# Kernel tuning notes

Hardware: AMD Instinct MI355X
Metric: run time of the kernel (lower is better)

## Reference

```python
import jax, jax.numpy as jnp
import numpy as np

B, N, P, HID = 1024, 30, 16, 128
NR = N * (N - 1)          # 870 directed edges
DR, DE, DO, NT = 3, 5, 6, 5


def _lin(x, w, b):
    return x @ w.T + b


def setup_inputs() -> dict:
    key = jax.random.key(0)
    ks = jax.random.split(key, 24)

    def w(k, o, i):
        return jax.random.normal(k, (o, i), jnp.float32) * 0.05

    def bias(k, o):
        return jax.random.normal(k, (o,), jnp.float32) * 0.05

    return {
        "x": jax.random.normal(ks[0], (B, N, P), jnp.float32),
        "RR": jax.random.normal(ks[1], (B, N, NR), jnp.float32),
        "RS": jax.random.normal(ks[2], (B, N, NR), jnp.float32),
        "RA": jax.random.normal(ks[3], (B, DR, NR), jnp.float32),
        "fr1_w": w(ks[4], HID, 2 * P + DR), "fr1_b": bias(ks[5], HID),
        "fr2_w": w(ks[6], HID // 2, HID),   "fr2_b": bias(ks[7], HID // 2),
        "fr3_w": w(ks[8], DE, HID // 2),    "fr3_b": bias(ks[9], DE),
        "fo1_w": w(ks[10], HID, P + DE),    "fo1_b": bias(ks[11], HID),
        "fo2_w": w(ks[12], HID // 2, HID),  "fo2_b": bias(ks[13], HID // 2),
        "fo3_w": w(ks[14], DO, HID // 2),   "fo3_b": bias(ks[15], DO),
        "fc1_w": w(ks[16], HID, DO * N),    "fc1_b": bias(ks[17], HID),
        "fc2_w": w(ks[18], HID // 2, HID),  "fc2_b": bias(ks[19], HID // 2),
        "fc3_w": w(ks[20], NT, HID // 2),   "fc3_b": bias(ks[21], NT),
    }


def reference(x, RR, RS, RA,
              fr1_w, fr1_b, fr2_w, fr2_b, fr3_w, fr3_b,
              fo1_w, fo1_b, fo2_w, fo2_b, fo3_w, fo3_b,
              fc1_w, fc1_b, fc2_w, fc2_b, fc3_w, fc3_b):
    xt = jnp.swapaxes(x, 1, 2)                       # [B, P, N]
    Orr = jnp.einsum('bpn,bnr->bpr', xt, RR)          # [B, P, Nr]
    Ors = jnp.einsum('bpn,bnr->bpr', xt, RS)          # [B, P, Nr]
    Bm = jnp.concatenate([Orr, Ors, RA], axis=1)      # [B, 2P+Dr, Nr]
    Bm = jnp.swapaxes(Bm, 1, 2)                       # [B, Nr, 2P+Dr]
    h = jax.nn.relu(_lin(Bm, fr1_w, fr1_b))
    h = jax.nn.relu(_lin(h, fr2_w, fr2_b))
    E = jax.nn.relu(_lin(h, fr3_w, fr3_b))            # [B, Nr, De]
    Ebar = jnp.einsum('bre,bnr->ben', E, RR)          # E^T @ RR^T -> [B, De, N]
    C = jnp.concatenate([xt, Ebar], axis=1)           # [B, P+De, N]
    C = jnp.swapaxes(C, 1, 2)                         # [B, N, P+De]
    h = jax.nn.relu(_lin(C, fo1_w, fo1_b))
    h = jax.nn.relu(_lin(h, fo2_w, fo2_b))
    O = jax.nn.relu(_lin(h, fo3_w, fo3_b))            # [B, N, Do]
    f = O.reshape(O.shape[0], -1)                     # [B, Do*N]
    f = jax.nn.relu(_lin(f, fc1_w, fc1_b))
    f = jax.nn.relu(_lin(f, fc2_w, fc2_b))
    return _lin(f, fc3_w, fc3_b)                      # [B, n_targets]
```

## Files before the change

kernel.cpp:

```cpp
#include <hip/hip_runtime.h>

#define B_ 1024
#define N_ 30
#define P_ 16
#define NR_ 870
#define DR_ 3
#define DE_ 5
#define DO_ 6
#define NT_ 5

typedef unsigned short ushort_t;
typedef __attribute__((ext_vector_type(8))) short short8_t;
typedef __attribute__((ext_vector_type(4))) float f32x4;

union Frag { short8_t v; ushort_t u[8]; unsigned int d[4]; };

__device__ __forceinline__ float bf2f(ushort_t u) {
    union { unsigned int i; float f; } v; v.i = ((unsigned int)u) << 16; return v.f;
}
__device__ __forceinline__ ushort_t f2bf(float f) {
    union { float f; unsigned int i; } v; v.f = f;
    unsigned int x = v.i;
    return (ushort_t)((x + 0x7FFFu + ((x >> 16) & 1u)) >> 16);
}
__device__ __forceinline__ void split(float v, ushort_t& h, ushort_t& l) {
    h = f2bf(v);
    float r = v - bf2f(h);
    l = f2bf(r);
}
__device__ __forceinline__ unsigned int cvtpk(float a, float b) {
    unsigned int r;
    asm("v_cvt_pk_bf16_f32 %0, %1, %2" : "=v"(r) : "v"(a), "v"(b));
    return r;
}
__device__ __forceinline__ void split2(float a, float b,
                                       unsigned int& h, unsigned int& l) {
    h = cvtpk(a, b);
    union { unsigned int i; float f; } x0, x1;
    x0.i = h << 16; x1.i = h & 0xFFFF0000u;
    l = cvtpk(a - x0.f, b - x1.f);
}
__device__ __forceinline__ f32x4 mfma(short8_t a, short8_t b, f32x4 c) {
    return __builtin_amdgcn_mfma_f32_16x16x32_bf16(a, b, c, 0, 0, 0);
}

__global__ __launch_bounds__(256) void k_prep(
    const float* __restrict__ x,  const float* __restrict__ w1,
    const float* __restrict__ w2, const float* __restrict__ wo1,
    const float* __restrict__ wo2,
    ushort_t* __restrict__ xAh,  ushort_t* __restrict__ xAl,
    ushort_t* __restrict__ w1h,  ushort_t* __restrict__ w1l,
    ushort_t* __restrict__ w2h,  ushort_t* __restrict__ w2l,
    ushort_t* __restrict__ wo1h, ushort_t* __restrict__ wo1l,
    ushort_t* __restrict__ wo2h, ushort_t* __restrict__ wo2l)
{
    const int blk = blockIdx.x, tid = threadIdx.x;
    if (blk < 1024) {
        int b = blk;
        for (int idx = tid; idx < 512; idx += 256) {
            int lane = idx >> 3, j = idx & 7;
            int p = lane & 15, n = (lane >> 4) * 8 + j;
            float v = (n < N_) ? x[(b * N_ + n) * P_ + p] : 0.f;
            ushort_t h_, l_; split(v, h_, l_);
            xAh[b * 512 + idx] = h_; xAl[b * 512 + idx] = l_;
        }
    } else if (blk == 1024) {
        for (int idx = tid; idx < 16 * 512; idx += 256) {
            int f = idx >> 9, eps = idx & 511;
            int lane = eps >> 3, j = eps & 7;
            int mt = f >> 1, kt = f & 1;
            int m = mt * 16 + (lane & 15);
            int k = kt * 32 + (lane >> 4) * 8 + j;
            float v = (k < 35) ? w1[m * 35 + k] : 0.f;
            ushort_t h_, l_; split(v, h_, l_);
            w1h[idx] = h_; w1l[idx] = l_;
        }
    } else if (blk == 1025) {
        for (int idx = tid; idx < 16 * 512; idx += 256) {
            int f = idx >> 9, eps = idx & 511;
            int lane = eps >> 3, j = eps & 7;
            int mt = f >> 2, kt = f & 3;
            int m = mt * 16 + (lane & 15);
            int k = kt * 32 + (lane >> 4) * 8 + j;
            float v = w2[m * 128 + k];
            ushort_t h_, l_; split(v, h_, l_);
            w2h[idx] = h_; w2l[idx] = l_;
        }
    } else if (blk == 1026) {
        for (int idx = tid; idx < 8 * 512; idx += 256) {
            int f = idx >> 9, eps = idx & 511;
            int lane = eps >> 3, j = eps & 7;
            int m = f * 16 + (lane & 15);
            int k = (lane >> 4) * 8 + j;
            float v = (k < 21) ? wo1[m * 21 + k] : 0.f;
            ushort_t h_, l_; split(v, h_, l_);
            wo1h[idx] = h_; wo1l[idx] = l_;
        }
    } else {
        for (int idx = tid; idx < 16 * 512; idx += 256) {
            int f = idx >> 9, eps = idx & 511;
            int lane = eps >> 3, j = eps & 7;
            int mt = f >> 2, kt = f & 3;
            int m = mt * 16 + (lane & 15);
            int k = kt * 32 + (lane >> 4) * 8 + j;
            float v = wo2[m * 128 + k];
            ushort_t h_, l_; split(v, h_, l_);
            wo2h[idx] = h_; wo2l[idx] = l_;
        }
    }
}

__global__ __launch_bounds__(256) void k_edge(
    const float* __restrict__ RR, const float* __restrict__ RS,
    const float* __restrict__ RA,
    const float* __restrict__ b1, const float* __restrict__ b2,
    const float* __restrict__ w3, const float* __restrict__ b3,
    const ushort_t* __restrict__ xAh, const ushort_t* __restrict__ xAl,
    const ushort_t* __restrict__ w1h, const ushort_t* __restrict__ w1l,
    const ushort_t* __restrict__ w2h, const ushort_t* __restrict__ w2l,
    float* __restrict__ Ebar)
{
    const int b   = blockIdx.y;
    const int r0  = blockIdx.x * 64;
    const int tid = threadIdx.x;
    const int lane = tid & 63;
    const int wv   = tid >> 6;
    const int l15  = lane & 15;
    const int q    = lane >> 4;

    __shared__ union {
        ushort_t aT[2][64][72];
        float    h2T[64][68];
    } u1;
    __shared__ ushort_t h1T[2][64][72];
    __shared__ float Ee[64][6];
    __shared__ float b1s[128], b2s[64];

    if (tid < 128) b1s[tid] = b1[tid];
    if (tid < 64)  b2s[tid] = b2[tid];

    const int eloc = wv * 16 + l15;
    const int r = r0 + eloc;
    const bool rvalid = (r < NR_);
    const int rc = rvalid ? r : NR_ - 1;

    {
        Frag xh, xl;
        xh.v = ((const short8_t*)xAh)[b * 64 + lane];
        xl.v = ((const short8_t*)xAl)[b * 64 + lane];

        float vr[8], vs[8];
        #pragma unroll
        for (int j = 0; j < 8; ++j) {
            int n = q * 8 + j;
            vr[j] = (n < N_) ? RR[(b * N_ + n) * NR_ + rc] : 0.f;
            vs[j] = (n < N_) ? RS[(b * N_ + n) * NR_ + rc] : 0.f;
        }
        Frag rrh, rrl, rsh, rsl;
        #pragma unroll
        for (int d0 = 0; d0 < 4; ++d0) {
            split2(vr[2*d0], vr[2*d0+1], rrh.d[d0], rrl.d[d0]);
            split2(vs[2*d0], vs[2*d0+1], rsh.d[d0], rsl.d[d0]);
        }

        f32x4 aR = {0.f,0.f,0.f,0.f}, aS = {0.f,0.f,0.f,0.f};
        aR = mfma(xh.v, rrh.v, aR); aR = mfma(xl.v, rrh.v, aR); aR = mfma(xh.v, rrl.v, aR);
        aS = mfma(xh.v, rsh.v, aS); aS = mfma(xl.v, rsh.v, aS); aS = mfma(xh.v, rsl.v, aS);

        uint4 z = {0u,0u,0u,0u};
        *(uint4*)&u1.aT[0][eloc][32 + q * 8] = z;
        *(uint4*)&u1.aT[1][eloc][32 + q * 8] = z;

        unsigned int h01, h23, l01, l23;
        split2(aR[0], aR[1], h01, l01); split2(aR[2], aR[3], h23, l23);
        { uint2 hh = {h01, h23}, ll = {l01, l23};
          *(uint2*)&u1.aT[0][eloc][q * 4] = hh;
          *(uint2*)&u1.aT[1][eloc][q * 4] = ll; }
        split2(aS[0], aS[1], h01, l01); split2(aS[2], aS[3], h23, l23);
        { uint2 hh = {h01, h23}, ll = {l01, l23};
          *(uint2*)&u1.aT[0][eloc][16 + q * 4] = hh;
          *(uint2*)&u1.aT[1][eloc][16 + q * 4] = ll; }

        if (q < DR_) {
            float v = rvalid ? RA[(b * DR_ + q) * NR_ + r] : 0.f;
            ushort_t h_, l_; split(v, h_, l_);
            u1.aT[0][eloc][32 + q] = h_;
            u1.aT[1][eloc][32 + q] = l_;
        }
    }
    __syncthreads();

    short8_t W2hf[4], W2lf[4];
    #pragma unroll
    for (int kt = 0; kt < 4; ++kt) {
        W2hf[kt] = ((const short8_t*)w2h)[(wv * 4 + kt) * 64 + lane];
        W2lf[kt] = ((const short8_t*)w2l)[(wv * 4 + kt) * 64 + lane];
    }
    f32x4 acc2[4];
    #pragma unroll
    for (int et = 0; et < 4; ++et) acc2[et] = (f32x4){0.f,0.f,0.f,0.f};

    #pragma unroll
    for (int hf = 0; hf < 2; ++hf) {
        {
            const int mt = hf * 4 + wv;
            short8_t W1hf_[2], W1lf_[2];
            #pragma unroll
            for (int kt = 0; kt < 2; ++kt) {
                W1hf_[kt] = ((const short8_t*)w1h)[(mt * 2 + kt) * 64 + lane];
                W1lf_[kt] = ((const short8_t*)w1l)[(mt * 2 + kt) * 64 + lane];
            }
            #pragma unroll
            for (int et = 0; et < 4; ++et) {
                int e = et * 16 + l15;
                f32x4 acc = {0.f,0.f,0.f,0.f};
                #pragma unroll
                for (int kt = 0; kt < 2; ++kt) {
                    short8_t Bh = *(const short8_t*)&u1.aT[0][e][kt * 32 + q * 8];
                    short8_t Bl = *(const short8_t*)&u1.aT[1][e][kt * 32 + q * 8];
                    acc = mfma(W1hf_[kt], Bh, acc);
                    acc = mfma(W1lf_[kt], Bh, acc);
                    acc = mfma(W1hf_[kt], Bl, acc);
                }
                float hv0 = fmaxf(acc[0] + b1s[mt * 16 + q * 4 + 0], 0.f);
                float hv1 = fmaxf(acc[1] + b1s[mt * 16 + q * 4 + 1], 0.f);
                float hv2 = fmaxf(acc[2] + b1s[mt * 16 + q * 4 + 2], 0.f);
                float hv3 = fmaxf(acc[3] + b1s[mt * 16 + q * 4 + 3], 0.f);
                unsigned int d01, d23, e01, e23;
                split2(hv0, hv1, d01, e01); split2(hv2, hv3, d23, e23);
                uint2 hh = {d01, d23}, ll = {e01, e23};
                *(uint2*)&h1T[0][e][wv * 16 + q * 4] = hh;
                *(uint2*)&h1T[1][e][wv * 16 + q * 4] = ll;
            }
        }
        __syncthreads();

        #pragma unroll
        for (int et = 0; et < 4; ++et) {
            int e = et * 16 + l15;
            #pragma unroll
            for (int ktl = 0; ktl < 2; ++ktl) {
                short8_t bh = *(const short8_t*)&h1T[0][e][ktl * 32 + q * 8];
                short8_t bl = *(const short8_t*)&h1T[1][e][ktl * 32 + q * 8];
                acc2[et] = mfma(W2hf[hf * 2 + ktl], bh, acc2[et]);
                acc2[et] = mfma(W2lf[hf * 2 + ktl], bh, acc2[et]);
                acc2[et] = mfma(W2hf[hf * 2 + ktl], bl, acc2[et]);
            }
        }
        if (hf == 1) {
            #pragma unroll
            for (int et = 0; et < 4; ++et) {
                int e = et * 16 + l15;
                float4 st;
                st.x = fmaxf(acc2[et][0] + b2s[wv * 16 + q * 4 + 0], 0.f);
                st.y = fmaxf(acc2[et][1] + b2s[wv * 16 + q * 4 + 1], 0.f);
                st.z = fmaxf(acc2[et][2] + b2s[wv * 16 + q * 4 + 2], 0.f);
                st.w = fmaxf(acc2[et][3] + b2s[wv * 16 + q * 4 + 3], 0.f);
                *(float4*)&u1.h2T[e][wv * 16 + q * 4] = st;
            }
        }
        __syncthreads();
    }

    for (int it = tid; it < 64 * DE_; it += 256) {
        int e = it / DE_, i = it - e * DE_;
        float s = b3[i];
        const float* wr = w3 + i * 64;
        #pragma unroll
        for (int k = 0; k < 64; k += 4) {
            float4 hv = *(const float4*)&u1.h2T[e][k];
            float4 wv4 = *(const float4*)&wr[k];
            s += hv.x * wv4.x + hv.y * wv4.y + hv.z * wv4.z + hv.w * wv4.w;
        }
        Ee[e][i] = ((r0 + e) < NR_) ? fmaxf(s, 0.f) : 0.f;
    }
    __syncthreads();

    if (tid < DE_ * N_) {
        int i = tid / N_, n = tid - i * N_;
        const float* pr = &RR[(b * N_ + n) * NR_ + r0];
        const int emax = (NR_ - r0 < 64) ? (NR_ - r0) : 64;
        float s = 0.f;
        for (int e = 0; e < emax; ++e) s += Ee[e][i] * pr[e];
        atomicAdd(&Ebar[(b * DE_ + i) * N_ + n], s);
    }
}

__global__ __launch_bounds__(256) void k_nodef(
    const float* __restrict__ x, const float* __restrict__ Ebar,
    const float* __restrict__ bo1, const float* __restrict__ bo2,
    const float* __restrict__ wo3, const float* __restrict__ bo3,
    const ushort_t* __restrict__ wo1h, const ushort_t* __restrict__ wo1l,
    const ushort_t* __restrict__ wo2h, const ushort_t* __restrict__ wo2l,
    const float* __restrict__ wc1, const float* __restrict__ bc1,
    const float* __restrict__ wc2, const float* __restrict__ bc2,
    const float* __restrict__ wc3, const float* __restrict__ bc3,
    float* __restrict__ out)
{
    const int b0 = blockIdx.x * 2;
    const int tid = threadIdx.x;
    const int lane = tid & 63;
    const int wv = tid >> 6;
    const int l15 = lane & 15;
    const int q = lane >> 4;

    __shared__ union {
        ushort_t cT[2][64][40];
        struct { float fs[2][184]; float h1s[2][128]; float h2s[2][64]; } f;
    } u2n;
    __shared__ ushort_t h1T[2][64][136];
    __shared__ float h2T[64][68];
    __shared__ float b1s[128], b2s[64];

    if (tid < 128) b1s[tid] = bo1[tid];
    if (tid < 64)  b2s[tid] = bo2[tid];

    for (int idx = tid; idx < 64 * 32; idx += 256) {
        int c = idx >> 5, k = idx & 31;
        int bb = c >> 5, n = c & 31;
        float v = 0.f;
        if (n < N_) {
            if (k < 16)      v = x[((b0 + bb) * N_ + n) * P_ + k];
            else if (k < 21) v = Ebar[((b0 + bb) * DE_ + (k - 16)) * N_ + n];
        }
        ushort_t h_, l_; split(v, h_, l_);
        u2n.cT[0][c][k] = h_; u2n.cT[1][c][k] = l_;
    }
    __syncthreads();

    {
        short8_t Wh[2], Wl[2];
        #pragma unroll
        for (int mi = 0; mi < 2; ++mi) {
            int mt = wv + mi * 4;
            Wh[mi] = ((const short8_t*)wo1h)[mt * 64 + lane];
            Wl[mi] = ((const short8_t*)wo1l)[mt * 64 + lane];
        }
        #pragma unroll
        for (int et = 0; et < 4; ++et) {
            int c = et * 16 + l15;
            short8_t bh = *(const short8_t*)&u2n.cT[0][c][q * 8];
            short8_t bl = *(const short8_t*)&u2n.cT[1][c][q * 8];
            #pragma unroll
            for (int mi = 0; mi < 2; ++mi) {
                int mt = wv + mi * 4;
                f32x4 acc = {0.f,0.f,0.f,0.f};
                acc = mfma(Wh[mi], bh, acc);
                acc = mfma(Wl[mi], bh, acc);
                acc = mfma(Wh[mi], bl, acc);
                float hv0 = fmaxf(acc[0] + b1s[mt * 16 + q * 4 + 0], 0.f);
                float hv1 = fmaxf(acc[1] + b1s[mt * 16 + q * 4 + 1], 0.f);
                float hv2 = fmaxf(acc[2] + b1s[mt * 16 + q * 4 + 2], 0.f);
                float hv3 = fmaxf(acc[3] + b1s[mt * 16 + q * 4 + 3], 0.f);
                unsigned int d01, d23, e01, e23;
                split2(hv0, hv1, d01, e01); split2(hv2, hv3, d23, e23);
                uint2 hh = {d01, d23}, ll = {e01, e23};
                *(uint2*)&h1T[0][c][mt * 16 + q * 4] = hh;
                *(uint2*)&h1T[1][c][mt * 16 + q * 4] = ll;
            }
        }
    }
    __syncthreads();

    {
        short8_t Wh[4], Wl[4];
        #pragma unroll
        for (int kt = 0; kt < 4; ++kt) {
            Wh[kt] = ((const short8_t*)wo2h)[(wv * 4 + kt) * 64 + lane];
            Wl[kt] = ((const short8_t*)wo2l)[(wv * 4 + kt) * 64 + lane];
        }
        #pragma unroll
        for (int et = 0; et < 4; ++et) {
            int c = et * 16 + l15;
            f32x4 acc = {0.f,0.f,0.f,0.f};
            #pragma unroll
            for (int kt = 0; kt < 4; ++kt) {
                short8_t bh = *(const short8_t*)&h1T[0][c][kt * 32 + q * 8];
                short8_t bl = *(const short8_t*)&h1T[1][c][kt * 32 + q * 8];
                acc = mfma(Wh[kt], bh, acc);
                acc = mfma(Wl[kt], bh, acc);
                acc = mfma(Wh[kt], bl, acc);
            }
            float4 st;
            st.x = fmaxf(acc[0] + b2s[wv * 16 + q * 4 + 0], 0.f);
            st.y = fmaxf(acc[1] + b2s[wv * 16 + q * 4 + 1], 0.f);
            st.z = fmaxf(acc[2] + b2s[wv * 16 + q * 4 + 2], 0.f);
            st.w = fmaxf(acc[3] + b2s[wv * 16 + q * 4 + 3], 0.f);
            *(float4*)&h2T[c][wv * 16 + q * 4] = st;
        }
    }
    __syncthreads();

    for (int it = tid; it < 384; it += 256) {
        int c = it / DO_, i = it - c * DO_;
        if (c < 64) {
            int bb = c >> 5, n = c & 31;
            if (n < N_) {
                float s = bo3[i];
                const float* wr = wo3 + i * 64;
                #pragma unroll
                for (int k = 0; k < 64; k += 4) {
                    float4 hv = *(const float4*)&h2T[c][k];
                    float4 wv4 = *(const float4*)&wr[k];
                    s += hv.x * wv4.x + hv.y * wv4.y + hv.z * wv4.z + hv.w * wv4.w;
                }
                u2n.f.fs[bb][n * DO_ + i] = fmaxf(s, 0.f);
            }
        }
    }
    __syncthreads();

    {
        int bl = tid >> 7, j = tid & 127;
        const float* wr = wc1 + j * 180;
        float s = bc1[j];
        #pragma unroll 5
        for (int k = 0; k < 180; k += 4) {
            float4 wv4 = *(const float4*)&wr[k];
            s += u2n.f.fs[bl][k] * wv4.x + u2n.f.fs[bl][k + 1] * wv4.y
               + u2n.f.fs[bl][k + 2] * wv4.z + u2n.f.fs[bl][k + 3] * wv4.w;
        }
        u2n.f.h1s[bl][j] = fmaxf(s, 0.f);
    }
    __syncthreads();

    if (tid < 128) {
        int bl = tid >> 6, j = tid & 63;
        const float* wr = wc2 + j * 128;
        float s = bc2[j];
        #pragma unroll 4
        for (int k = 0; k < 128; k += 4) {
            float4 wv4 = *(const float4*)&wr[k];
            s += u2n.f.h1s[bl][k] * wv4.x + u2n.f.h1s[bl][k + 1] * wv4.y
               + u2n.f.h1s[bl][k + 2] * wv4.z + u2n.f.h1s[bl][k + 3] * wv4.w;
        }
        u2n.f.h2s[bl][j] = fmaxf(s, 0.f);
    }
    __syncthreads();

    if (tid < 10) {
        int bl = tid / 5, t = tid - bl * 5;
        const float* wr = wc3 + t * 64;
        float s = bc3[t];
        #pragma unroll
        for (int k = 0; k < 64; k += 4) {
            float4 wv4 = *(const float4*)&wr[k];
            s += u2n.f.h2s[bl][k] * wv4.x + u2n.f.h2s[bl][k + 1] * wv4.y
               + u2n.f.h2s[bl][k + 2] * wv4.z + u2n.f.h2s[bl][k + 3] * wv4.w;
        }
        out[(b0 + bl) * NT_ + t] = s;
    }
}

extern "C" void kernel_launch(void* const* d_in, const int* in_sizes, int n_in,
                              void* d_out, int out_size, void* d_ws, size_t ws_size,
                              hipStream_t stream)
{
    const float* x    = (const float*)d_in[0];
    const float* RR   = (const float*)d_in[1];
    const float* RS   = (const float*)d_in[2];
    const float* RA   = (const float*)d_in[3];
    const float* fr1w = (const float*)d_in[4];
    const float* fr1b = (const float*)d_in[5];
    const float* fr2w = (const float*)d_in[6];
    const float* fr2b = (const float*)d_in[7];
    const float* fr3w = (const float*)d_in[8];
    const float* fr3b = (const float*)d_in[9];
    const float* fo1w = (const float*)d_in[10];
    const float* fo1b = (const float*)d_in[11];
    const float* fo2w = (const float*)d_in[12];
    const float* fo2b = (const float*)d_in[13];
    const float* fo3w = (const float*)d_in[14];
    const float* fo3b = (const float*)d_in[15];
    const float* fc1w = (const float*)d_in[16];
    const float* fc1b = (const float*)d_in[17];
    const float* fc2w = (const float*)d_in[18];
    const float* fc2b = (const float*)d_in[19];
    const float* fc3w = (const float*)d_in[20];
    const float* fc3b = (const float*)d_in[21];
    float* out = (float*)d_out;

    float* Ebar = (float*)d_ws;
    ushort_t* base = (ushort_t*)(Ebar + B_ * DE_ * N_);
    ushort_t* xAh  = base;             ushort_t* xAl  = xAh  + 1024 * 512;
    ushort_t* w1h  = xAl  + 1024*512;  ushort_t* w1l  = w1h  + 16 * 512;
    ushort_t* w2h  = w1l  + 16*512;    ushort_t* w2l  = w2h  + 16 * 512;
    ushort_t* wo1h = w2l  + 16*512;    ushort_t* wo1l = wo1h + 8 * 512;
    ushort_t* wo2h = wo1l + 8*512;     ushort_t* wo2l = wo2h + 16 * 512;

    hipMemsetAsync(Ebar, 0, (size_t)B_ * DE_ * N_ * sizeof(float), stream);

    k_prep<<<1028, 256, 0, stream>>>(x, fr1w, fr2w, fo1w, fo2w,
                                     xAh, xAl, w1h, w1l, w2h, w2l,
                                     wo1h, wo1l, wo2h, wo2l);

    dim3 g1(14, B_);
    k_edge<<<g1, 256, 0, stream>>>(RR, RS, RA, fr1b, fr2b, fr3w, fr3b,
                                   xAh, xAl, w1h, w1l, w2h, w2l, Ebar);
    k_nodef<<<B_ / 2, 256, 0, stream>>>(x, Ebar, fo1b, fo2b, fo3w, fo3b,
                                        wo1h, wo1l, wo2h, wo2l,
                                        fc1w, fc1b, fc2w, fc2b, fc3w, fc3b, out);
}
```

Before: 549.9 us.

## Shrink edge-kernel LDS via scalar RA term and split node kernel per batch

The edge kernel no longer pads the 35-wide first-layer input to 64 for the MFMA. It runs a single 32-wide K tile and adds the three RA columns with scalar FMAs from fp32 weights. This shrinks the staging buffer and lets h1T share a union with h2T, so a barrier is added before h2T overwrites it. The node kernel now processes one batch per block instead of two, halving its shared memory, and both kernels get launch bounds requesting higher occupancy. The aim is to cut MFMA work and LDS footprint to raise occupancy, at the cost of an extra barrier and less per-block work in the node kernel.

```diff
diff --git a/kernel.cpp b/kernel.cpp
--- a/kernel.cpp
+++ b/kernel.cpp
@@ -110,9 +110,9 @@
     }
 }
 
-__global__ __launch_bounds__(256) void k_edge(
+__global__ __launch_bounds__(256, 5) void k_edge(
     const float* __restrict__ RR, const float* __restrict__ RS,
-    const float* __restrict__ RA,
+    const float* __restrict__ RA, const float* __restrict__ w1f,
     const float* __restrict__ b1, const float* __restrict__ b2,
     const float* __restrict__ w3, const float* __restrict__ b3,
     const ushort_t* __restrict__ xAh, const ushort_t* __restrict__ xAl,
@@ -128,12 +128,13 @@
     const int l15  = lane & 15;
     const int q    = lane >> 4;
 
+    __shared__ ushort_t aT[2][64][40];
     __shared__ union {
-        ushort_t aT[2][64][72];
+        ushort_t h1T[2][64][72];
         float    h2T[64][68];
-    } u1;
-    __shared__ ushort_t h1T[2][64][72];
+    } u2;
     __shared__ float Ee[64][6];
+    __shared__ float raT[64][4];
     __shared__ float b1s[128], b2s[64];
 
     if (tid < 128) b1s[tid] = b1[tid];
@@ -167,26 +168,18 @@
         aR = mfma(xh.v, rrh.v, aR); aR = mfma(xl.v, rrh.v, aR); aR = mfma(xh.v, rrl.v, aR);
         aS = mfma(xh.v, rsh.v, aS); aS = mfma(xl.v, rsh.v, aS); aS = mfma(xh.v, rsl.v, aS);
 
-        uint4 z = {0u,0u,0u,0u};
-        *(uint4*)&u1.aT[0][eloc][32 + q * 8] = z;
-        *(uint4*)&u1.aT[1][eloc][32 + q * 8] = z;
-
         unsigned int h01, h23, l01, l23;
         split2(aR[0], aR[1], h01, l01); split2(aR[2], aR[3], h23, l23);
         { uint2 hh = {h01, h23}, ll = {l01, l23};
-          *(uint2*)&u1.aT[0][eloc][q * 4] = hh;
-          *(uint2*)&u1.aT[1][eloc][q * 4] = ll; }
+          *(uint2*)&aT[0][eloc][q * 4] = hh;
+          *(uint2*)&aT[1][eloc][q * 4] = ll; }
         split2(aS[0], aS[1], h01, l01); split2(aS[2], aS[3], h23, l23);
         { uint2 hh = {h01, h23}, ll = {l01, l23};
-          *(uint2*)&u1.aT[0][eloc][16 + q * 4] = hh;
-          *(uint2*)&u1.aT[1][eloc][16 + q * 4] = ll; }
-
-        if (q < DR_) {
-            float v = rvalid ? RA[(b * DR_ + q) * NR_ + r] : 0.f;
-            ushort_t h_, l_; split(v, h_, l_);
-            u1.aT[0][eloc][32 + q] = h_;
-            u1.aT[1][eloc][32 + q] = l_;
-        }
+          *(uint2*)&aT[0][eloc][16 + q * 4] = hh;
+          *(uint2*)&aT[1][eloc][16 + q * 4] = ll; }
+
+        if (q < DR_)
+            raT[eloc][q] = rvalid ? RA[(b * DR_ + q) * NR_ + r] : 0.f;
     }
     __syncthreads();
 
@@ -204,33 +197,39 @@
     for (int hf = 0; hf < 2; ++hf) {
         {
             const int mt = hf * 4 + wv;
-            short8_t W1hf_[2], W1lf_[2];
-            #pragma unroll
-            for (int kt = 0; kt < 2; ++kt) {
-                W1hf_[kt] = ((const short8_t*)w1h)[(mt * 2 + kt) * 64 + lane];
-                W1lf_[kt] = ((const short8_t*)w1l)[(mt * 2 + kt) * 64 + lane];
+            short8_t W1h0 = ((const short8_t*)w1h)[(mt * 2 + 0) * 64 + lane];
+            short8_t W1l0 = ((const short8_t*)w1l)[(mt * 2 + 0) * 64 + lane];
+            float w1c[4][3];
+            #pragma unroll
+            for (int c = 0; c < 4; ++c) {
+                int row = mt * 16 + q * 4 + c;
+                w1c[c][0] = w1f[row * 35 + 32];
+                w1c[c][1] = w1f[row * 35 + 33];
+                w1c[c][2] = w1f[row * 35 + 34];
             }
             #pragma unroll
             for (int et = 0; et < 4; ++et) {
                 int e = et * 16 + l15;
                 f32x4 acc = {0.f,0.f,0.f,0.f};
-                #pragma unroll
-                for (int kt = 0; kt < 2; ++kt) {
-                    short8_t Bh = *(const short8_t*)&u1.aT[0][e][kt * 32 + q * 8];
-                    short8_t Bl = *(const short8_t*)&u1.aT[1][e][kt * 32 + q * 8];
-                    acc = mfma(W1hf_[kt], Bh, acc);
-                    acc = mfma(W1lf_[kt], Bh, acc);
-                    acc = mfma(W1hf_[kt], Bl, acc);
-                }
-                float hv0 = fmaxf(acc[0] + b1s[mt * 16 + q * 4 + 0], 0.f);
-                float hv1 = fmaxf(acc[1] + b1s[mt * 16 + q * 4 + 1], 0.f);
-                float hv2 = fmaxf(acc[2] + b1s[mt * 16 + q * 4 + 2], 0.f);
-                float hv3 = fmaxf(acc[3] + b1s[mt * 16 + q * 4 + 3], 0.f);
+                short8_t Bh = *(const short8_t*)&aT[0][e][q * 8];
+                short8_t Bl = *(const short8_t*)&aT[1][e][q * 8];
+                acc = mfma(W1h0, Bh, acc);
+                acc = mfma(W1l0, Bh, acc);
+                acc = mfma(W1h0, Bl, acc);
+                float ra0 = raT[e][0], ra1 = raT[e][1], ra2 = raT[e][2];
+                float hv0 = fmaxf(acc[0] + b1s[mt*16 + q*4 + 0]
+                                  + w1c[0][0]*ra0 + w1c[0][1]*ra1 + w1c[0][2]*ra2, 0.f);
+                float hv1 = fmaxf(acc[1] + b1s[mt*16 + q*4 + 1]
+                                  + w1c[1][0]*ra0 + w1c[1][1]*ra1 + w1c[1][2]*ra2, 0.f);
+                float hv2 = fmaxf(acc[2] + b1s[mt*16 + q*4 + 2]
+                                  + w1c[2][0]*ra0 + w1c[2][1]*ra1 + w1c[2][2]*ra2, 0.f);
+                float hv3 = fmaxf(acc[3] + b1s[mt*16 + q*4 + 3]
+                                  + w1c[3][0]*ra0 + w1c[3][1]*ra1 + w1c[3][2]*ra2, 0.f);
                 unsigned int d01, d23, e01, e23;
                 split2(hv0, hv1, d01, e01); split2(hv2, hv3, d23, e23);
                 uint2 hh = {d01, d23}, ll = {e01, e23};
-                *(uint2*)&h1T[0][e][wv * 16 + q * 4] = hh;
-                *(uint2*)&h1T[1][e][wv * 16 + q * 4] = ll;
+                *(uint2*)&u2.h1T[0][e][wv * 16 + q * 4] = hh;
+                *(uint2*)&u2.h1T[1][e][wv * 16 + q * 4] = ll;
             }
         }
         __syncthreads();
@@ -240,14 +239,15 @@
             int e = et * 16 + l15;
             #pragma unroll
             for (int ktl = 0; ktl < 2; ++ktl) {
-                short8_t bh = *(const short8_t*)&h1T[0][e][ktl * 32 + q * 8];
-                short8_t bl = *(const short8_t*)&h1T[1][e][ktl * 32 + q * 8];
+                short8_t bh = *(const short8_t*)&u2.h1T[0][e][ktl * 32 + q * 8];
+                short8_t bl = *(const short8_t*)&u2.h1T[1][e][ktl * 32 + q * 8];
                 acc2[et] = mfma(W2hf[hf * 2 + ktl], bh, acc2[et]);
                 acc2[et] = mfma(W2lf[hf * 2 + ktl], bh, acc2[et]);
                 acc2[et] = mfma(W2hf[hf * 2 + ktl], bl, acc2[et]);
             }
         }
         if (hf == 1) {
+            __syncthreads();
             #pragma unroll
             for (int et = 0; et < 4; ++et) {
                 int e = et * 16 + l15;
@@ -256,7 +256,7 @@
                 st.y = fmaxf(acc2[et][1] + b2s[wv * 16 + q * 4 + 1], 0.f);
                 st.z = fmaxf(acc2[et][2] + b2s[wv * 16 + q * 4 + 2], 0.f);
                 st.w = fmaxf(acc2[et][3] + b2s[wv * 16 + q * 4 + 3], 0.f);
-                *(float4*)&u1.h2T[e][wv * 16 + q * 4] = st;
+                *(float4*)&u2.h2T[e][wv * 16 + q * 4] = st;
             }
         }
         __syncthreads();
@@ -268,7 +268,7 @@
         const float* wr = w3 + i * 64;
         #pragma unroll
         for (int k = 0; k < 64; k += 4) {
-            float4 hv = *(const float4*)&u1.h2T[e][k];
+            float4 hv = *(const float4*)&u2.h2T[e][k];
             float4 wv4 = *(const float4*)&wr[k];
             s += hv.x * wv4.x + hv.y * wv4.y + hv.z * wv4.z + hv.w * wv4.w;
         }
@@ -286,7 +286,7 @@
     }
 }
 
-__global__ __launch_bounds__(256) void k_nodef(
+__global__ __launch_bounds__(256, 5) void k_nodef(
     const float* __restrict__ x, const float* __restrict__ Ebar,
     const float* __restrict__ bo1, const float* __restrict__ bo2,
     const float* __restrict__ wo3, const float* __restrict__ bo3,
@@ -297,7 +297,7 @@
     const float* __restrict__ wc3, const float* __restrict__ bc3,
     float* __restrict__ out)
 {
-    const int b0 = blockIdx.x * 2;
+    const int b = blockIdx.x;
     const int tid = threadIdx.x;
     const int lane = tid & 63;
     const int wv = tid >> 6;
@@ -305,26 +305,25 @@
     const int q = lane >> 4;
 
     __shared__ union {
-        ushort_t cT[2][64][40];
-        struct { float fs[2][184]; float h1s[2][128]; float h2s[2][64]; } f;
-    } u2n;
-    __shared__ ushort_t h1T[2][64][136];
-    __shared__ float h2T[64][68];
+        ushort_t cT[2][32][40];
+        struct { float fs[192]; float h1s[128]; float h2s[64]; } f;
+    } u;
+    __shared__ ushort_t h1T[2][32][136];
+    __shared__ float h2T[32][68];
     __shared__ float b1s[128], b2s[64];
 
     if (tid < 128) b1s[tid] = bo1[tid];
     if (tid < 64)  b2s[tid] = bo2[tid];
 
-    for (int idx = tid; idx < 64 * 32; idx += 256) {
+    for (int idx = tid; idx < 32 * 32; idx += 256) {
         int c = idx >> 5, k = idx & 31;
-        int bb = c >> 5, n = c & 31;
         float v = 0.f;
-        if (n < N_) {
-            if (k < 16)      v = x[((b0 + bb) * N_ + n) * P_ + k];
-            else if (k < 21) v = Ebar[((b0 + bb) * DE_ + (k - 16)) * N_ + n];
+        if (c < N_) {
+            if (k < 16)      v = x[(b * N_ + c) * P_ + k];
+            else if (k < 21) v = Ebar[(b * DE_ + (k - 16)) * N_ + c];
         }
         ushort_t h_, l_; split(v, h_, l_);
-        u2n.cT[0][c][k] = h_; u2n.cT[1][c][k] = l_;
+        u.cT[0][c][k] = h_; u.cT[1][c][k] = l_;
     }
     __syncthreads();
 
@@ -337,10 +336,10 @@
             Wl[mi] = ((const short8_t*)wo1l)[mt * 64 + lane];
         }
         #pragma unroll
-        for (int et = 0; et < 4; ++et) {
+        for (int et = 0; et < 2; ++et) {
             int c = et * 16 + l15;
-            short8_t bh = *(const short8_t*)&u2n.cT[0][c][q * 8];
-            short8_t bl = *(const short8_t*)&u2n.cT[1][c][q * 8];
+            short8_t bh = *(const short8_t*)&u.cT[0][c][q * 8];
+            short8_t bl = *(const short8_t*)&u.cT[1][c][q * 8];
             #pragma unroll
             for (int mi = 0; mi < 2; ++mi) {
                 int mt = wv + mi * 4;
@@ -370,7 +369,7 @@
             Wl[kt] = ((const short8_t*)wo2l)[(wv * 4 + kt) * 64 + lane];
         }
         #pragma unroll
-        for (int et = 0; et < 4; ++et) {
+        for (int et = 0; et < 2; ++et) {
             int c = et * 16 + l15;
             f32x4 acc = {0.f,0.f,0.f,0.f};
             #pragma unroll
@@ -391,64 +390,58 @@
     }
     __syncthreads();
 
-    for (int it = tid; it < 384; it += 256) {
-        int c = it / DO_, i = it - c * DO_;
-        if (c < 64) {
-            int bb = c >> 5, n = c & 31;
-            if (n < N_) {
-                float s = bo3[i];
-                const float* wr = wo3 + i * 64;
-                #pragma unroll
-                for (int k = 0; k < 64; k += 4) {
-                    float4 hv = *(const float4*)&h2T[c][k];
-                    float4 wv4 = *(const float4*)&wr[k];
-                    s += hv.x * wv4.x + hv.y * wv4.y + hv.z * wv4.z + hv.w * wv4.w;
-                }
-                u2n.f.fs[bb][n * DO_ + i] = fmaxf(s, 0.f);
-            }
-        }
-    }
-    __syncthreads();
-
-    {
-        int bl = tid >> 7, j = tid & 127;
-        const float* wr = wc1 + j * 180;
-        float s = bc1[j];
+    if (tid < N_ * DO_ + 12) {
+        int c = tid / DO_, i = tid - c * DO_;
+        if (c < N_) {
+            float s = bo3[i];
+            const float* wr = wo3 + i * 64;
+            #pragma unroll
+            for (int k = 0; k < 64; k += 4) {
+                float4 hv = *(const float4*)&h2T[c][k];
+                float4 wv4 = *(const float4*)&wr[k];
+                s += hv.x * wv4.x + hv.y * wv4.y + hv.z * wv4.z + hv.w * wv4.w;
+            }
+            u.f.fs[c * DO_ + i] = fmaxf(s, 0.f);
+        }
+    }
+    __syncthreads();
+
+    if (tid < 128) {
+        const float* wr = wc1 + tid * 180;
+        float s = bc1[tid];
         #pragma unroll 5
         for (int k = 0; k < 180; k += 4) {
             float4 wv4 = *(const float4*)&wr[k];
-            s += u2n.f.fs[bl][k] * wv4.x + u2n.f.fs[bl][k + 1] * wv4.y
-               + u2n.f.fs[bl][k + 2] * wv4.z + u2n.f.fs[bl][k + 3] * wv4.w;
-        }
-        u2n.f.h1s[bl][j] = fmaxf(s, 0.f);
-    }
-    __syncthreads();
-
-    if (tid < 128) {
-        int bl = tid >> 6, j = tid & 63;
-        const float* wr = wc2 + j * 128;
-        float s = bc2[j];
+            s += u.f.fs[k] * wv4.x + u.f.fs[k + 1] * wv4.y
+               + u.f.fs[k + 2] * wv4.z + u.f.fs[k + 3] * wv4.w;
+        }
+        u.f.h1s[tid] = fmaxf(s, 0.f);
+    }
+    __syncthreads();
+
+    if (tid < 64) {
+        const float* wr = wc2 + tid * 128;
+        float s = bc2[tid];
         #pragma unroll 4
         for (int k = 0; k < 128; k += 4) {
             float4 wv4 = *(const float4*)&wr[k];
-            s += u2n.f.h1s[bl][k] * wv4.x + u2n.f.h1s[bl][k + 1] * wv4.y
-               + u2n.f.h1s[bl][k + 2] * wv4.z + u2n.f.h1s[bl][k + 3] * wv4.w;
-        }
-        u2n.f.h2s[bl][j] = fmaxf(s, 0.f);
-    }
-    __syncthreads();
-
-    if (tid < 10) {
-        int bl = tid / 5, t = tid - bl * 5;
-        const float* wr = wc3 + t * 64;
-        float s = bc3[t];
+            s += u.f.h1s[k] * wv4.x + u.f.h1s[k + 1] * wv4.y
+               + u.f.h1s[k + 2] * wv4.z + u.f.h1s[k + 3] * wv4.w;
+        }
+        u.f.h2s[tid] = fmaxf(s, 0.f);
+    }
+    __syncthreads();
+
+    if (tid < NT_) {
+        const float* wr = wc3 + tid * 64;
+        float s = bc3[tid];
         #pragma unroll
         for (int k = 0; k < 64; k += 4) {
             float4 wv4 = *(const float4*)&wr[k];
-            s += u2n.f.h2s[bl][k] * wv4.x + u2n.f.h2s[bl][k + 1] * wv4.y
-               + u2n.f.h2s[bl][k + 2] * wv4.z + u2n.f.h2s[bl][k + 3] * wv4.w;
-        }
-        out[(b0 + bl) * NT_ + t] = s;
+            s += u.f.h2s[k] * wv4.x + u.f.h2s[k + 1] * wv4.y
+               + u.f.h2s[k + 2] * wv4.z + u.f.h2s[k + 3] * wv4.w;
+        }
+        out[b * NT_ + tid] = s;
     }
 }
 
@@ -495,9 +488,9 @@
                                      wo1h, wo1l, wo2h, wo2l);
 
     dim3 g1(14, B_);
-    k_edge<<<g1, 256, 0, stream>>>(RR, RS, RA, fr1b, fr2b, fr3w, fr3b,
+    k_edge<<<g1, 256, 0, stream>>>(RR, RS, RA, fr1w, fr1b, fr2b, fr3w, fr3b,
                                    xAh, xAl, w1h, w1l, w2h, w2l, Ebar);
-    k_nodef<<<B_ / 2, 256, 0, stream>>>(x, Ebar, fo1b, fo2b, fo3w, fo3b,
-                                        wo1h, wo1l, wo2h, wo2l,
-                                        fc1w, fc1b, fc2w, fc2b, fc3w, fc3b, out);
-}
+    k_nodef<<<B_, 256, 0, stream>>>(x, Ebar, fo1b, fo2b, fo3w, fo3b,
+                                    wo1h, wo1l, wo2h, wo2l,
+                                    fc1w, fc1b, fc2w, fc2b, fc3w, fc3b, out);
+}
```

Measured after the change: 578.3 us. +5.2%, slower.
